# Kernel tuning notes

Hardware: AMD Instinct MI355X
Metric: run time of the kernel (lower is better)

## Reference

```python
import jax, jax.numpy as jnp
import numpy as np

EPS = 1e-5

def _fake_quant(w, axis):
    # symmetric int8 fake-quant with straight-through estimator
    s = jnp.max(jnp.abs(w), axis=axis, keepdims=True) / 127.0 + 1e-8
    q = jnp.clip(jnp.round(w / s), -127.0, 127.0) * s
    return w + jax.lax.stop_gradient(q - w)

def _qconv1x1(x, w, b):
    # x: [B, C_in, Q, H, W]; w: [C_out, C_in] (1x1 kernel); weight fake-quantized
    wq = _fake_quant(w, axis=1)
    return jnp.einsum('bcqhw,oc->boqhw', x, wq) + b[None, :, None, None, None]

def setup_inputs() -> dict:
    key = jax.random.key(0)
    ks = jax.random.split(key, 12)
    B, C, Q, H, W = 8, 256, 4, 40, 40
    x = jax.random.normal(ks[0], (B, C, Q, H, W), dtype=jnp.float32)
    scale = 1.0 / np.sqrt(C)
    Wq = jax.random.normal(ks[1], (C, C), dtype=jnp.float32) * scale
    Wk = jax.random.normal(ks[2], (C, C), dtype=jnp.float32) * scale
    Wv = jax.random.normal(ks[3], (C, C), dtype=jnp.float32) * scale
    Wp = jax.random.normal(ks[4], (C, C), dtype=jnp.float32) * scale
    bq = jnp.zeros((C,), jnp.float32)
    bk = jnp.zeros((C,), jnp.float32)
    bv = jnp.zeros((C,), jnp.float32)
    bp = jnp.zeros((C,), jnp.float32)
    gamma = jnp.ones((C,), jnp.float32)
    beta = jnp.zeros((C,), jnp.float32)
    return {"x": x, "Wq": Wq, "bq": bq, "Wk": Wk, "bk": bk,
            "Wv": Wv, "bv": bv, "Wp": Wp, "bp": bp,
            "gamma": gamma, "beta": beta}

def reference(x, Wq, bq, Wk, bk, Wv, bv, Wp, bp, gamma, beta):
    B, C, Q, H, W = x.shape
    q = _qconv1x1(x, Wq, bq)
    k = _qconv1x1(x, Wk, bk)
    v = _qconv1x1(x, Wv, bv)
    # per-rotation channel attention: [B, Q=4, C, H*W]
    qh = q.reshape(B, C, Q, H * W).transpose(0, 2, 1, 3)
    kh = k.reshape(B, C, Q, H * W).transpose(0, 2, 1, 3)
    vh = v.reshape(B, C, Q, H * W).transpose(0, 2, 1, 3)
    scale = 1.0 / jnp.sqrt(jnp.float32(C // 4))
    attn = jnp.einsum('bqcn,bqdn->bqcd', qh, kh) * scale  # [B,4,C,C]
    attn = jax.nn.softmax(attn, axis=-1)
    out = jnp.einsum('bqcd,bqdn->bqcn', attn, vh)  # [B,4,C,HW]
    out = out.transpose(0, 2, 1, 3).reshape(B, C, Q, H, W)
    out = _qconv1x1(out, Wp, bp)
    # IQBN: per-channel batchnorm with int8 fake-quantized gamma
    mean = jnp.mean(out, axis=(0, 2, 3, 4), keepdims=True)
    var = jnp.var(out, axis=(0, 2, 3, 4), keepdims=True)
    g = _fake_quant(gamma, axis=None)[None, :, None, None, None]
    b = beta[None, :, None, None, None]
    out = (out - mean) * jax.lax.rsqrt(var + EPS) * g + b
    return out
```

## Files before the change

kernel.cpp:

```cpp
#include <hip/hip_runtime.h>
#include <math.h>

#define BB 8
#define CCH 256
#define QQ 4
#define NN 1600
#define BQN 32
#define SP 51200
#define EPSF 1e-5f

typedef __attribute__((ext_vector_type(8))) short bf16x8;
typedef __attribute__((ext_vector_type(4))) float f32x4;

static __device__ inline ushort f2bf(float f) {
  union { float f; unsigned u; } v; v.f = f;
  return (ushort)((v.u + 0x7fffu + ((v.u >> 16) & 1u)) >> 16);
}
static __device__ inline float bf2f(ushort u) {
  union { unsigned u; float f; } v; v.u = ((unsigned)u) << 16;
  return v.f;
}
static __device__ inline void gld16(const ushort* g, ushort* l) {
  __builtin_amdgcn_global_load_lds(
      (const __attribute__((address_space(1))) unsigned int*)g,
      (__attribute__((address_space(3))) unsigned int*)l, 16, 0, 0);
}

__global__ void quant_weights_kernel(const float* Wq, const float* Wk,
                                     const float* Wv, const float* Wp,
                                     const float* gamma,
                                     ushort* wq, ushort* wk, ushort* wvT, ushort* wp,
                                     float* gq, float* r) {
  __shared__ float red[256];
  int blk = blockIdx.x;
  int tid = threadIdx.x;
  if (blk < 1024) {
    int mat = blk >> 8;
    int row = blk & 255;
    const float* W = (mat == 0) ? Wq : (mat == 1) ? Wk : (mat == 2) ? Wv : Wp;
    float w = W[row * 256 + tid];
    red[tid] = fabsf(w);
    __syncthreads();
    for (int s = 128; s > 0; s >>= 1) {
      if (tid < s) red[tid] = fmaxf(red[tid], red[tid + s]);
      __syncthreads();
    }
    float s = red[0] / 127.0f + 1e-8f;
    float q = fminf(fmaxf(rintf(w / s), -127.0f), 127.0f) * s;
    ushort qb = f2bf(q);
    if (mat == 0)      wq[row * 256 + tid] = qb;
    else if (mat == 1) wk[row * 256 + tid] = qb;
    else if (mat == 2) wvT[tid * 256 + row] = qb;
    else               wp[row * 256 + tid] = qb;
  } else {
    float g = gamma[tid];
    red[tid] = fabsf(g);
    __syncthreads();
    for (int s = 128; s > 0; s >>= 1) {
      if (tid < s) red[tid] = fmaxf(red[tid], red[tid + s]);
      __syncthreads();
    }
    float s = red[0] / 127.0f + 1e-8f;
    gq[tid] = fminf(fmaxf(rintf(g / s), -127.0f), 127.0f) * s;
    for (int i = tid; i < BQN * 256; i += 256) r[i] = 0.f;
  }
}

__global__ __launch_bounds__(256)
void prep_kernel(const float* __restrict__ x, ushort* __restrict__ xb,
                 ushort* __restrict__ xT, float* __restrict__ r) {
  int bqi = blockIdx.z, b = bqi >> 2, q = bqi & 3;
  int s0 = blockIdx.x * 64, c0 = blockIdx.y * 64;
  __shared__ ushort lT[64 * 66];
  int tid = threadIdx.x;
  int c = tid >> 2, nch = (tid & 3) * 16;
  const float* xp = x + ((size_t)(b * CCH + c0 + c) * QQ + q) * NN + s0 + nch;
  union { ushort u[16]; int4 v[2]; } nb;
  float s = 0.f;
#pragma unroll
  for (int j = 0; j < 4; j++) {
    float4 f = ((const float4*)xp)[j];
    s += f.x + f.y + f.z + f.w;
    nb.u[j * 4 + 0] = f2bf(f.x);
    nb.u[j * 4 + 1] = f2bf(f.y);
    nb.u[j * 4 + 2] = f2bf(f.z);
    nb.u[j * 4 + 3] = f2bf(f.w);
    lT[c * 66 + nch + j * 4 + 0] = nb.u[j * 4 + 0];
    lT[c * 66 + nch + j * 4 + 1] = nb.u[j * 4 + 1];
    lT[c * 66 + nch + j * 4 + 2] = nb.u[j * 4 + 2];
    lT[c * 66 + nch + j * 4 + 3] = nb.u[j * 4 + 3];
  }
  ushort* xbp = xb + (size_t)bqi * (CCH * NN) + (size_t)(c0 + c) * NN + s0 + nch;
  *(int4*)xbp = nb.v[0];
  *((int4*)xbp + 1) = nb.v[1];
  s += __shfl_down(s, 2);
  s += __shfl_down(s, 1);
  if ((tid & 3) == 0) atomicAdd(&r[bqi * 256 + c0 + c], s);
  __syncthreads();
  int n = tid >> 2, cch = (tid & 3) * 16;
  union { ushort u[16]; int4 v[2]; } o;
#pragma unroll
  for (int i = 0; i < 16; i++) o.u[i] = lT[(cch + i) * 66 + n];
  ushort* dst = xT + (size_t)(bqi * NN + s0 + n) * CCH + c0 + cch;
  *(int4*)dst = o.v[0];
  *((int4*)dst + 1) = o.v[1];
}

__global__ __launch_bounds__(256)
void gram_kernel(const ushort* __restrict__ xb, ushort* __restrict__ Gh,
                 ushort* __restrict__ Gl) {
  __shared__ __align__(16) char smem[32768];
  float* lC = (float*)smem;
  int z = blockIdx.z;
  int mBase = blockIdx.y * 128, nBase = blockIdx.x * 128;
  int tid = threadIdx.x, wave = tid >> 6, lane = tid & 63;
  int wm = wave >> 1, wn = wave & 1;
  int col = lane & 15, quad = lane >> 4;
  int srow = tid >> 2, skc = (tid & 3) * 8;
  const ushort* X = xb + (size_t)z * (CCH * NN);
  const ushort* gA  = X + (size_t)(mBase + srow) * NN + skc;
  const ushort* gA2 = gA + (size_t)64 * NN;
  const ushort* gB  = X + (size_t)(nBase + srow) * NN + skc;
  const ushort* gB2 = gB + (size_t)64 * NN;
  ushort* sA1[2]; ushort* sA2[2]; ushort* sB1[2]; ushort* sB2[2];
#pragma unroll
  for (int b = 0; b < 2; b++) {
    ushort* lAb = (ushort*)(smem + b * 16384);
    ushort* lBb = (ushort*)(smem + b * 16384 + 8192);
    sA1[b] = &lAb[srow * 32 + skc];
    sA2[b] = &lAb[(64 + srow) * 32 + skc];
    sB1[b] = &lBb[srow * 32 + skc];
    sB2[b] = &lBb[(64 + srow) * 32 + skc];
  }
  f32x4 acc[4][4];
#pragma unroll
  for (int i = 0; i < 4; i++)
#pragma unroll
    for (int j = 0; j < 4; j++) acc[i][j] = (f32x4){0.f, 0.f, 0.f, 0.f};

  const int nIter = NN / 32;
  gld16(gA, sA1[0]); gld16(gA2, sA2[0]); gld16(gB, sB1[0]); gld16(gB2, sB2[0]);
  for (int it = 0; it < nIter; ++it) {
    int cur = it & 1;
    __syncthreads();
    if (it + 1 < nIter) {
      int kt = (it + 1) << 5, nxt = cur ^ 1;
      gld16(gA + kt, sA1[nxt]); gld16(gA2 + kt, sA2[nxt]);
      gld16(gB + kt, sB1[nxt]); gld16(gB2 + kt, sB2[nxt]);
    }
    const ushort* lAc = (const ushort*)(smem + cur * 16384);
    const ushort* lBc = (const ushort*)(smem + cur * 16384 + 8192);
    bf16x8 af[4], bfr[4];
#pragma unroll
    for (int i = 0; i < 4; i++)
      af[i] = *(const bf16x8*)&lAc[(wm * 64 + i * 16 + col) * 32 + quad * 8];
#pragma unroll
    for (int j = 0; j < 4; j++)
      bfr[j] = *(const bf16x8*)&lBc[(wn * 64 + j * 16 + col) * 32 + quad * 8];
#pragma unroll
    for (int i = 0; i < 4; i++)
#pragma unroll
      for (int j = 0; j < 4; j++)
        acc[i][j] = __builtin_amdgcn_mfma_f32_16x16x32_bf16(af[i], bfr[j], acc[i][j], 0, 0, 0);
  }
  __syncthreads();
  float* lCw = lC + wave * 16 * 68;
  int mW = mBase + wm * 64, nW = nBase + wn * 64;
#pragma unroll
  for (int i = 0; i < 4; i++) {
#pragma unroll
    for (int j = 0; j < 4; j++)
#pragma unroll
      for (int rg = 0; rg < 4; rg++)
        lCw[(quad * 4 + rg) * 68 + j * 16 + col] = acc[i][j][rg];
    int mrow0 = mW + i * 16;
    int rr = lane & 15, cc = lane >> 4;
    union { ushort u[16]; int4 v[2]; } oh, ol;
#pragma unroll
    for (int t = 0; t < 16; t++) {
      float vfl = lCw[rr * 68 + cc * 16 + t];
      ushort hh = f2bf(vfl);
      oh.u[t] = hh;
      ol.u[t] = f2bf(vfl - bf2f(hh));
    }
    size_t off = (size_t)z * 65536 + (size_t)(mrow0 + rr) * 256 + nW + cc * 16;
    *(int4*)(Gh + off) = oh.v[0];
    *((int4*)(Gh + off) + 1) = oh.v[1];
    *(int4*)(Gl + off) = ol.v[0];
    *((int4*)(Gl + off) + 1) = ol.v[1];
  }
}

template<int MODE>
__global__ __launch_bounds__(256)
void gemm256(const ushort* __restrict__ A, long sA, const ushort* __restrict__ A2,
             const ushort* __restrict__ B, long sB, const ushort* __restrict__ B2,
             void* __restrict__ C1, void* __restrict__ C2, long sC) {
  __shared__ __align__(16) char smem[24576];
  ushort* lA = (ushort*)smem;
  ushort* lB = (ushort*)(smem + 8192);
  ushort* lX = (ushort*)(smem + 16384);
  float* lC = (float*)smem;
  int z = blockIdx.z;
  int mBase = blockIdx.y * 128, nBase = blockIdx.x * 128;
  int tid = threadIdx.x, wave = tid >> 6, lane = tid & 63;
  int wm = wave >> 1, wn = wave & 1;
  int col = lane & 15, quad = lane >> 4;
  int srow = tid >> 2, skc = (tid & 3) * 8;
  const ushort* Az = A + (size_t)z * sA;
  const ushort* Bz = B + (size_t)z * sB;
  const ushort* gA  = Az + (size_t)(mBase + srow) * 256 + skc;
  const ushort* gA2r = gA + 64 * 256;
  const ushort* gB  = Bz + (size_t)(nBase + srow) * 256 + skc;
  const ushort* gB2r = gB + 64 * 256;
  const ushort* gX = nullptr;
  const ushort* gX2 = nullptr;
  if (MODE == 0) {
    const ushort* Xz = B2 + (size_t)z * sB;
    gX = Xz + (size_t)(nBase + srow) * 256 + skc;
    gX2 = gX + 64 * 256;
  } else if (MODE == 1) {
    const ushort* Xz = A2 + (size_t)z * sA;
    gX = Xz + (size_t)(mBase + srow) * 256 + skc;
    gX2 = gX + 64 * 256;
  }
  ushort* dA1 = &lA[srow * 32 + skc]; ushort* dA2 = &lA[(64 + srow) * 32 + skc];
  ushort* dB1 = &lB[srow * 32 + skc]; ushort* dB2 = &lB[(64 + srow) * 32 + skc];
  ushort* dX1 = &lX[srow * 32 + skc]; ushort* dX2 = &lX[(64 + srow) * 32 + skc];

  f32x4 acc[4][4];
#pragma unroll
  for (int i = 0; i < 4; i++)
#pragma unroll
    for (int j = 0; j < 4; j++) acc[i][j] = (f32x4){0.f, 0.f, 0.f, 0.f};

  for (int kt = 0; kt < 256; kt += 32) {
    __syncthreads();
    gld16(gA + kt, dA1); gld16(gA2r + kt, dA2);
    gld16(gB + kt, dB1); gld16(gB2r + kt, dB2);
    if (MODE <= 1) { gld16(gX + kt, dX1); gld16(gX2 + kt, dX2); }
    __syncthreads();
    bf16x8 af[4], bfr[4], xf[4];
#pragma unroll
    for (int i = 0; i < 4; i++)
      af[i] = *(const bf16x8*)&lA[(wm * 64 + i * 16 + col) * 32 + quad * 8];
#pragma unroll
    for (int j = 0; j < 4; j++)
      bfr[j] = *(const bf16x8*)&lB[(wn * 64 + j * 16 + col) * 32 + quad * 8];
    if (MODE == 0) {
#pragma unroll
      for (int j = 0; j < 4; j++)
        xf[j] = *(const bf16x8*)&lX[(wn * 64 + j * 16 + col) * 32 + quad * 8];
    } else if (MODE == 1) {
#pragma unroll
      for (int i = 0; i < 4; i++)
        xf[i] = *(const bf16x8*)&lX[(wm * 64 + i * 16 + col) * 32 + quad * 8];
    }
#pragma unroll
    for (int i = 0; i < 4; i++)
#pragma unroll
      for (int j = 0; j < 4; j++) {
        acc[i][j] = __builtin_amdgcn_mfma_f32_16x16x32_bf16(af[i], bfr[j], acc[i][j], 0, 0, 0);
        if (MODE == 0)
          acc[i][j] = __builtin_amdgcn_mfma_f32_16x16x32_bf16(af[i], xf[j], acc[i][j], 0, 0, 0);
        else if (MODE == 1)
          acc[i][j] = __builtin_amdgcn_mfma_f32_16x16x32_bf16(xf[i], bfr[j], acc[i][j], 0, 0, 0);
      }
  }
  __syncthreads();
  float* lCw = lC + wave * 16 * 68;
  int mW = mBase + wm * 64, nW = nBase + wn * 64;
#pragma unroll
  for (int i = 0; i < 4; i++) {
#pragma unroll
    for (int j = 0; j < 4; j++)
#pragma unroll
      for (int rg = 0; rg < 4; rg++)
        lCw[(quad * 4 + rg) * 68 + j * 16 + col] = acc[i][j][rg];
    int mrow0 = mW + i * 16;
    int rr = lane & 15, cc = lane >> 4;
    if (MODE == 0) {
      union { ushort u[16]; int4 v[2]; } oh, ol;
#pragma unroll
      for (int t = 0; t < 16; t++) {
        float vfl = lCw[rr * 68 + cc * 16 + t];
        ushort hh = f2bf(vfl);
        oh.u[t] = hh;
        ol.u[t] = f2bf(vfl - bf2f(hh));
      }
      size_t off = (size_t)z * sC + (size_t)(mrow0 + rr) * 256 + nW + cc * 16;
      *(int4*)((ushort*)C1 + off) = oh.v[0];
      *((int4*)((ushort*)C1 + off) + 1) = oh.v[1];
      *(int4*)((ushort*)C2 + off) = ol.v[0];
      *((int4*)((ushort*)C2 + off) + 1) = ol.v[1];
    } else if (MODE == 1) {
      float* C = (float*)C1 + (size_t)z * sC + (size_t)(mrow0 + rr) * 256 + nW + cc * 16;
#pragma unroll
      for (int v = 0; v < 4; v++) {
        float4 f;
        f.x = lCw[rr * 68 + cc * 16 + v * 4 + 0];
        f.y = lCw[rr * 68 + cc * 16 + v * 4 + 1];
        f.z = lCw[rr * 68 + cc * 16 + v * 4 + 2];
        f.w = lCw[rr * 68 + cc * 16 + v * 4 + 3];
        *(float4*)(C + v * 4) = f;
      }
    } else if (MODE == 2) {
      int n = nW + lane;
      union { ushort u[16]; int4 v[2]; } o;
#pragma unroll
      for (int t = 0; t < 16; t++) o.u[t] = f2bf(lCw[t * 68 + lane]);
      ushort* C = (ushort*)C1 + (size_t)z * sC + (size_t)n * 256 + mrow0;
      *(int4*)C = o.v[0];
      *((int4*)C + 1) = o.v[1];
    } else {
      union { ushort u[16]; int4 v[2]; } o;
#pragma unroll
      for (int t = 0; t < 16; t++) o.u[t] = f2bf(lCw[rr * 68 + cc * 16 + t]);
      ushort* C = (ushort*)C1 + (size_t)z * sC + (size_t)(mrow0 + rr) * 256 + nW + cc * 16;
      *(int4*)C = o.v[0];
      *((int4*)C + 1) = o.v[1];
    }
  }
}

__global__ void uv_kernel(const ushort* __restrict__ wq, const ushort* __restrict__ wk,
                          const float* __restrict__ r, float* __restrict__ u,
                          float* __restrict__ vv) {
  int bq = blockIdx.x, sel = blockIdx.y, c = threadIdx.x;
  const ushort* W = sel ? wk : wq;
  float s = 0.f;
  for (int i = 0; i < 256; i++) s += bf2f(W[c * 256 + i]) * r[bq * 256 + i];
  (sel ? vv : u)[bq * 256 + c] = s;
}

__global__ void softmax_kernel(const float* __restrict__ S, const float* __restrict__ u,
                               const float* __restrict__ vv, const float* __restrict__ bqv,
                               const float* __restrict__ bkv, const float* __restrict__ bvv,
                               ushort* __restrict__ P, float* __restrict__ pb) {
  int bi = blockIdx.x;
  int bq = bi >> 8, rw = bi & 255;
  int tid = threadIdx.x;
  size_t off = (size_t)bq * 65536 + (size_t)rw * 256 + tid;
  float bqc = bqv[rw], bkd = bkv[tid];
  float val = 0.125f * (S[off] + u[bq * 256 + rw] * bkd + bqc * vv[bq * 256 + tid]
                        + 1600.0f * bqc * bkd);
  __shared__ float red[256];
  red[tid] = val;
  __syncthreads();
  for (int s = 128; s > 0; s >>= 1) {
    if (tid < s) red[tid] = fmaxf(red[tid], red[tid + s]);
    __syncthreads();
  }
  float m = red[0];
  __syncthreads();
  float e = expf(val - m);
  red[tid] = e;
  __syncthreads();
  for (int s = 128; s > 0; s >>= 1) {
    if (tid < s) red[tid] += red[tid + s];
    __syncthreads();
  }
  float p = e / red[0];
  P[off] = f2bf(p);
  __syncthreads();
  red[tid] = p * bvv[tid];
  __syncthreads();
  for (int s = 128; s > 0; s >>= 1) {
    if (tid < s) red[tid] += red[tid + s];
    __syncthreads();
  }
  if (tid == 0) pb[bq * 256 + rw] = red[0];
}

__global__ void bo_kernel(const ushort* __restrict__ wp, const float* __restrict__ pb,
                          const float* __restrict__ bp, float* __restrict__ bo) {
  int bq = blockIdx.x, o = threadIdx.x;
  float s = bp[o];
  for (int c = 0; c < 256; c++) s += bf2f(wp[o * 256 + c]) * pb[bq * 256 + c];
  bo[bq * 256 + o] = s;
}

__global__ __launch_bounds__(256)
void final_kernel(const ushort* __restrict__ Tm, const ushort* __restrict__ xT,
                  const float* __restrict__ bo, float* __restrict__ out,
                  float* __restrict__ part) {
  __shared__ __align__(16) char smem[32768];
  float* lC = (float*)smem;
  __shared__ float psS[2][128];
  __shared__ float psS2[2][128];
  int z = blockIdx.z;
  int mBase = blockIdx.y * 128, nBase = blockIdx.x * 128;
  int tid = threadIdx.x, wave = tid >> 6, lane = tid & 63;
  int wm = wave >> 1, wn = wave & 1;
  int col = lane & 15, quad = lane >> 4;
  int srow = tid >> 2, skc = (tid & 3) * 8;
  const ushort* Az = Tm + (size_t)z * 65536;
  const ushort* Bz = xT + (size_t)z * (NN * 256);
  const ushort* gA  = Az + (size_t)(mBase + srow) * 256 + skc;
  const ushort* gA2 = gA + 64 * 256;
  int br1 = nBase + srow;      br1 = br1 < NN ? br1 : NN - 1;
  int br2 = nBase + 64 + srow; br2 = br2 < NN ? br2 : NN - 1;
  const ushort* gB  = Bz + (size_t)br1 * 256 + skc;
  const ushort* gB2 = Bz + (size_t)br2 * 256 + skc;
  ushort* sA1[2]; ushort* sA2[2]; ushort* sB1[2]; ushort* sB2[2];
#pragma unroll
  for (int b = 0; b < 2; b++) {
    ushort* lAb = (ushort*)(smem + b * 16384);
    ushort* lBb = (ushort*)(smem + b * 16384 + 8192);
    sA1[b] = &lAb[srow * 32 + skc];
    sA2[b] = &lAb[(64 + srow) * 32 + skc];
    sB1[b] = &lBb[srow * 32 + skc];
    sB2[b] = &lBb[(64 + srow) * 32 + skc];
  }
  f32x4 acc[4][4];
#pragma unroll
  for (int i = 0; i < 4; i++)
#pragma unroll
    for (int j = 0; j < 4; j++) acc[i][j] = (f32x4){0.f, 0.f, 0.f, 0.f};

  const int nIter = 8;
  gld16(gA, sA1[0]); gld16(gA2, sA2[0]); gld16(gB, sB1[0]); gld16(gB2, sB2[0]);
  for (int it = 0; it < nIter; ++it) {
    int cur = it & 1;
    __syncthreads();
    if (it + 1 < nIter) {
      int kt = (it + 1) << 5, nxt = cur ^ 1;
      gld16(gA + kt, sA1[nxt]); gld16(gA2 + kt, sA2[nxt]);
      gld16(gB + kt, sB1[nxt]); gld16(gB2 + kt, sB2[nxt]);
    }
    const ushort* lAc = (const ushort*)(smem + cur * 16384);
    const ushort* lBc = (const ushort*)(smem + cur * 16384 + 8192);
    bf16x8 af[4], bfr[4];
#pragma unroll
    for (int i = 0; i < 4; i++)
      af[i] = *(const bf16x8*)&lAc[(wm * 64 + i * 16 + col) * 32 + quad * 8];
#pragma unroll
    for (int j = 0; j < 4; j++)
      bfr[j] = *(const bf16x8*)&lBc[(wn * 64 + j * 16 + col) * 32 + quad * 8];
#pragma unroll
    for (int i = 0; i < 4; i++)
#pragma unroll
      for (int j = 0; j < 4; j++)
        acc[i][j] = __builtin_amdgcn_mfma_f32_16x16x32_bf16(af[i], bfr[j], acc[i][j], 0, 0, 0);
  }
  __syncthreads();
  float* lCw = lC + wave * 16 * 68;
  int mW = mBase + wm * 64, nW = nBase + wn * 64;
  int b = z >> 2, q = z & 3;
#pragma unroll
  for (int i = 0; i < 4; i++) {
#pragma unroll
    for (int j = 0; j < 4; j++)
#pragma unroll
      for (int rg = 0; rg < 4; rg++)
        lCw[(quad * 4 + rg) * 68 + j * 16 + col] = acc[i][j][rg];
    int mrow0 = mW + i * 16;
    int rr = lane & 15, cc = lane >> 4;
    int n0 = nW + cc * 16;
    float bi = bo[(size_t)z * 256 + mrow0 + rr];
    float ls = 0.f, ls2 = 0.f;
    if (n0 < NN) {
      float* C = out + (size_t)b * (CCH * QQ * NN)
               + (size_t)(mrow0 + rr) * (QQ * NN) + (size_t)q * NN + n0;
#pragma unroll
      for (int v = 0; v < 4; v++) {
        float4 f;
        f.x = lCw[rr * 68 + cc * 16 + v * 4 + 0] + bi;
        f.y = lCw[rr * 68 + cc * 16 + v * 4 + 1] + bi;
        f.z = lCw[rr * 68 + cc * 16 + v * 4 + 2] + bi;
        f.w = lCw[rr * 68 + cc * 16 + v * 4 + 3] + bi;
        *(float4*)(C + v * 4) = f;
        ls  += f.x + f.y + f.z + f.w;
        ls2 += f.x * f.x + f.y * f.y + f.z * f.z + f.w * f.w;
      }
    }
    ls  += __shfl_down(ls, 32);  ls  += __shfl_down(ls, 16);
    ls2 += __shfl_down(ls2, 32); ls2 += __shfl_down(ls2, 16);
    if (lane < 16) {
      psS[wn][wm * 64 + i * 16 + lane] = ls;
      psS2[wn][wm * 64 + i * 16 + lane] = ls2;
    }
  }
  __syncthreads();
  if (tid < 128) {
    float s  = psS[0][tid] + psS[1][tid];
    float s2 = psS2[0][tid] + psS2[1][tid];
    int slot = z * 13 + blockIdx.x;
    part[(size_t)slot * 256 + mBase + tid] = s;
    part[416 * 256 + (size_t)slot * 256 + mBase + tid] = s2;
  }
}

__global__ void stats2_kernel(const float* __restrict__ part, float* __restrict__ st) {
  int o = blockIdx.x;
  int tid = threadIdx.x;
  float s = 0.f, s2 = 0.f;
  for (int x = tid; x < 416; x += 256) {
    s  += part[(size_t)x * 256 + o];
    s2 += part[416 * 256 + (size_t)x * 256 + o];
  }
  __shared__ float rs[256], rs2[256];
  rs[tid] = s; rs2[tid] = s2;
  __syncthreads();
  for (int t = 128; t > 0; t >>= 1) {
    if (tid < t) { rs[tid] += rs[tid + t]; rs2[tid] += rs2[tid + t]; }
    __syncthreads();
  }
  if (tid == 0) {
    float inv = 1.0f / (float)(BQN * NN);
    float mean = rs[0] * inv;
    float var = rs2[0] * inv - mean * mean;
    st[o] = mean;
    st[CCH + o] = var;
  }
}

__global__ __launch_bounds__(256)
void bn_kernel(float* __restrict__ out, const float* __restrict__ st,
               const float* __restrict__ gq, const float* __restrict__ beta) {
  size_t i4 = (size_t)blockIdx.x * 256 + threadIdx.x;
  int o = (int)((i4 / 1600) & 255);
  float mean = st[o];
  float g = rsqrtf(st[CCH + o] + EPSF) * gq[o];
  float be = beta[o];
  float4 f = ((const float4*)out)[i4];
  f.x = (f.x - mean) * g + be;
  f.y = (f.y - mean) * g + be;
  f.z = (f.z - mean) * g + be;
  f.w = (f.w - mean) * g + be;
  ((float4*)out)[i4] = f;
}

extern "C" void kernel_launch(void* const* d_in, const int* in_sizes, int n_in,
                              void* d_out, int out_size, void* d_ws, size_t ws_size,
                              hipStream_t stream) {
  const float* x     = (const float*)d_in[0];
  const float* Wq    = (const float*)d_in[1];
  const float* bq    = (const float*)d_in[2];
  const float* Wk    = (const float*)d_in[3];
  const float* bk    = (const float*)d_in[4];
  const float* Wv    = (const float*)d_in[5];
  const float* bv    = (const float*)d_in[6];
  const float* Wp    = (const float*)d_in[7];
  const float* bp    = (const float*)d_in[8];
  const float* gamma = (const float*)d_in[9];
  const float* beta  = (const float*)d_in[10];
  float* out = (float*)d_out;

  ushort* h    = (ushort*)d_ws;
  ushort* wq   = h;
  ushort* wk   = wq + 65536;
  ushort* wp   = wk + 65536;
  ushort* wvT  = wp + 65536;
  ushort* xb   = wvT + 65536;
  ushort* xT   = xb + (size_t)BQN * CCH * NN;
  ushort* Gh   = xT + (size_t)BQN * CCH * NN;
  ushort* Gl   = Gh + (size_t)BQN * 65536;
  ushort* M1h  = Gl + (size_t)BQN * 65536;
  ushort* M1l  = M1h + (size_t)BQN * 65536;
  ushort* P    = M1l + (size_t)BQN * 65536;
  ushort* N1t  = P + (size_t)BQN * 65536;
  ushort* Tm   = N1t + (size_t)BQN * 65536;
  float*  S    = (float*)(Tm + (size_t)BQN * 65536);
  float*  r    = S + (size_t)BQN * 65536;
  float*  u    = r + 8192;
  float*  vv   = u + 8192;
  float*  pb   = vv + 8192;
  float*  bo   = pb + 8192;
  float*  gq   = bo + 8192;
  float*  st   = gq + 256;
  float*  part = st + 512;

  quant_weights_kernel<<<1025, 256, 0, stream>>>(Wq, Wk, Wv, Wp, gamma,
                                                 wq, wk, wvT, wp, gq, r);
  prep_kernel<<<dim3(NN / 64, CCH / 64, BQN), 256, 0, stream>>>(x, xb, xT, r);
  uv_kernel<<<dim3(BQN, 2), 256, 0, stream>>>(wq, wk, r, u, vv);
  gram_kernel<<<dim3(2, 2, BQN), 256, 0, stream>>>(xb, Gh, Gl);
  gemm256<0><<<dim3(2, 2, BQN), 256, 0, stream>>>(
      wq, 0, nullptr, Gh, 65536, Gl, M1h, M1l, 65536);
  gemm256<1><<<dim3(2, 2, BQN), 256, 0, stream>>>(
      M1h, 65536, M1l, wk, 0, nullptr, S, nullptr, 65536);
  softmax_kernel<<<BQN * CCH, 256, 0, stream>>>(S, u, vv, bq, bk, bv, P, pb);
  gemm256<2><<<dim3(2, 2, BQN), 256, 0, stream>>>(
      P, 65536, nullptr, wvT, 0, nullptr, N1t, nullptr, 65536);
  gemm256<3><<<dim3(2, 2, BQN), 256, 0, stream>>>(
      wp, 0, nullptr, N1t, 65536, nullptr, Tm, nullptr, 65536);
  bo_kernel<<<BQN, 256, 0, stream>>>(wp, pb, bp, bo);
  final_kernel<<<dim3(13, 2, BQN), 256, 0, stream>>>(Tm, xT, bo, out, part);
  stats2_kernel<<<CCH, 256, 0, stream>>>(part, st);
  bn_kernel<<<(BB * CCH * QQ * NN / 4) / 256, 256, 0, stream>>>(out, st, gq, beta);
}
```

Before: 285.9 us.

## Compute batchnorm stats analytically from Gram matrix and split Gram over K

Measured after the change: 314.5 us. +10.0%, slower.

```diff
diff --git a/kernel.cpp b/kernel.cpp
--- a/kernel.cpp
+++ b/kernel.cpp
@@ -30,7 +30,7 @@
                                      const float* Wv, const float* Wp,
                                      const float* gamma,
                                      ushort* wq, ushort* wk, ushort* wvT, ushort* wp,
-                                     float* gq, float* r) {
+                                     float* gq, float* r, float* diagacc, float* tracc) {
   __shared__ float red[256];
   int blk = blockIdx.x;
   int tid = threadIdx.x;
@@ -62,7 +62,9 @@
     }
     float s = red[0] / 127.0f + 1e-8f;
     gq[tid] = fminf(fmaxf(rintf(g / s), -127.0f), 127.0f) * s;
-    for (int i = tid; i < BQN * 256; i += 256) r[i] = 0.f;
+    for (int i = tid; i < BQN * 256; i += 256) {
+      r[i] = 0.f; diagacc[i] = 0.f; tracc[i] = 0.f;
+    }
   }
 }
 
@@ -80,15 +82,15 @@
 #pragma unroll
   for (int j = 0; j < 4; j++) {
     float4 f = ((const float4*)xp)[j];
-    s += f.x + f.y + f.z + f.w;
     nb.u[j * 4 + 0] = f2bf(f.x);
     nb.u[j * 4 + 1] = f2bf(f.y);
     nb.u[j * 4 + 2] = f2bf(f.z);
     nb.u[j * 4 + 3] = f2bf(f.w);
-    lT[c * 66 + nch + j * 4 + 0] = nb.u[j * 4 + 0];
-    lT[c * 66 + nch + j * 4 + 1] = nb.u[j * 4 + 1];
-    lT[c * 66 + nch + j * 4 + 2] = nb.u[j * 4 + 2];
-    lT[c * 66 + nch + j * 4 + 3] = nb.u[j * 4 + 3];
+#pragma unroll
+    for (int t = 0; t < 4; t++) {
+      s += bf2f(nb.u[j * 4 + t]);
+      lT[c * 66 + nch + j * 4 + t] = nb.u[j * 4 + t];
+    }
   }
   ushort* xbp = xb + (size_t)bqi * (CCH * NN) + (size_t)(c0 + c) * NN + s0 + nch;
   *(int4*)xbp = nb.v[0];
@@ -107,17 +109,18 @@
 }
 
 __global__ __launch_bounds__(256)
-void gram_kernel(const ushort* __restrict__ xb, ushort* __restrict__ Gh,
-                 ushort* __restrict__ Gl) {
+void gram_part_kernel(const ushort* __restrict__ xb, float* __restrict__ Gp) {
   __shared__ __align__(16) char smem[32768];
-  float* lC = (float*)smem;
   int z = blockIdx.z;
+  int bq = z & 31, chunk = z >> 5;
+  int kbase = chunk * 416;
+  int Kc = 1600 - kbase; if (Kc > 416) Kc = 416;
   int mBase = blockIdx.y * 128, nBase = blockIdx.x * 128;
   int tid = threadIdx.x, wave = tid >> 6, lane = tid & 63;
   int wm = wave >> 1, wn = wave & 1;
   int col = lane & 15, quad = lane >> 4;
   int srow = tid >> 2, skc = (tid & 3) * 8;
-  const ushort* X = xb + (size_t)z * (CCH * NN);
+  const ushort* X = xb + (size_t)bq * (CCH * NN) + kbase;
   const ushort* gA  = X + (size_t)(mBase + srow) * NN + skc;
   const ushort* gA2 = gA + (size_t)64 * NN;
   const ushort* gB  = X + (size_t)(nBase + srow) * NN + skc;
@@ -138,7 +141,7 @@
 #pragma unroll
     for (int j = 0; j < 4; j++) acc[i][j] = (f32x4){0.f, 0.f, 0.f, 0.f};
 
-  const int nIter = NN / 32;
+  int nIter = Kc >> 5;
   gld16(gA, sA1[0]); gld16(gA2, sA2[0]); gld16(gB, sB1[0]); gld16(gB2, sB2[0]);
   for (int it = 0; it < nIter; ++it) {
     int cur = it & 1;
@@ -163,31 +166,45 @@
       for (int j = 0; j < 4; j++)
         acc[i][j] = __builtin_amdgcn_mfma_f32_16x16x32_bf16(af[i], bfr[j], acc[i][j], 0, 0, 0);
   }
-  __syncthreads();
-  float* lCw = lC + wave * 16 * 68;
-  int mW = mBase + wm * 64, nW = nBase + wn * 64;
-#pragma unroll
-  for (int i = 0; i < 4; i++) {
+  float* G = Gp + (size_t)z * 65536;
+#pragma unroll
+  for (int i = 0; i < 4; i++)
 #pragma unroll
     for (int j = 0; j < 4; j++)
 #pragma unroll
-      for (int rg = 0; rg < 4; rg++)
-        lCw[(quad * 4 + rg) * 68 + j * 16 + col] = acc[i][j][rg];
-    int mrow0 = mW + i * 16;
-    int rr = lane & 15, cc = lane >> 4;
-    union { ushort u[16]; int4 v[2]; } oh, ol;
-#pragma unroll
-    for (int t = 0; t < 16; t++) {
-      float vfl = lCw[rr * 68 + cc * 16 + t];
-      ushort hh = f2bf(vfl);
-      oh.u[t] = hh;
-      ol.u[t] = f2bf(vfl - bf2f(hh));
-    }
-    size_t off = (size_t)z * 65536 + (size_t)(mrow0 + rr) * 256 + nW + cc * 16;
-    *(int4*)(Gh + off) = oh.v[0];
-    *((int4*)(Gh + off) + 1) = oh.v[1];
-    *(int4*)(Gl + off) = ol.v[0];
-    *((int4*)(Gl + off) + 1) = ol.v[1];
+      for (int rg = 0; rg < 4; rg++) {
+        int row = mBase + wm * 64 + i * 16 + quad * 4 + rg;
+        int cl  = nBase + wn * 64 + j * 16 + col;
+        G[row * 256 + cl] = acc[i][j][rg];
+      }
+}
+
+__global__ __launch_bounds__(256)
+void gram_reduce_kernel(const float* __restrict__ Gp, ushort* __restrict__ Gh,
+                        ushort* __restrict__ Gl) {
+  int bq = blockIdx.x, tid = threadIdx.x;
+  const size_t cs = (size_t)32 * 65536;
+  for (int k = 0; k < 32; k++) {
+    size_t f8 = (size_t)(tid + k * 256) * 8;
+    size_t base = (size_t)bq * 65536 + f8;
+    union { ushort u[8]; int4 v; } oh, ol;
+#pragma unroll
+    for (int t = 0; t < 8; t += 4) {
+      float4 a = *(const float4*)(Gp + base + t);
+      float4 b = *(const float4*)(Gp + cs + base + t);
+      float4 c = *(const float4*)(Gp + 2 * cs + base + t);
+      float4 d = *(const float4*)(Gp + 3 * cs + base + t);
+      float v0 = a.x + b.x + c.x + d.x;
+      float v1 = a.y + b.y + c.y + d.y;
+      float v2 = a.z + b.z + c.z + d.z;
+      float v3 = a.w + b.w + c.w + d.w;
+      ushort h0 = f2bf(v0), h1 = f2bf(v1), h2 = f2bf(v2), h3 = f2bf(v3);
+      oh.u[t] = h0; oh.u[t + 1] = h1; oh.u[t + 2] = h2; oh.u[t + 3] = h3;
+      ol.u[t] = f2bf(v0 - bf2f(h0)); ol.u[t + 1] = f2bf(v1 - bf2f(h1));
+      ol.u[t + 2] = f2bf(v2 - bf2f(h2)); ol.u[t + 3] = f2bf(v3 - bf2f(h3));
+    }
+    *(int4*)(Gh + base) = oh.v;
+    *(int4*)(Gl + base) = ol.v;
   }
 }
 
@@ -381,13 +398,120 @@
 }
 
 __global__ __launch_bounds__(256)
+void tgt_kernel(const ushort* __restrict__ Tm, const ushort* __restrict__ Gh,
+                const ushort* __restrict__ Gl, const float* __restrict__ r,
+                float* __restrict__ diagacc, float* __restrict__ tracc) {
+  __shared__ __align__(16) char smem[24576];
+  ushort* lA = (ushort*)smem;
+  ushort* lB = (ushort*)(smem + 8192);
+  ushort* lX = (ushort*)(smem + 16384);
+  float* lC = (float*)smem;
+  int z = blockIdx.z;
+  int mBase = blockIdx.y * 128, nBase = blockIdx.x * 128;
+  int tid = threadIdx.x, wave = tid >> 6, lane = tid & 63;
+  int wm = wave >> 1, wn = wave & 1;
+  int col = lane & 15, quad = lane >> 4;
+  int srow = tid >> 2, skc = (tid & 3) * 8;
+  const ushort* Az = Tm + (size_t)z * 65536;
+  const ushort* Bz = Gh + (size_t)z * 65536;
+  const ushort* Xz = Gl + (size_t)z * 65536;
+  const ushort* gA  = Az + (size_t)(mBase + srow) * 256 + skc;
+  const ushort* gA2r = gA + 64 * 256;
+  const ushort* gB  = Bz + (size_t)(nBase + srow) * 256 + skc;
+  const ushort* gB2r = gB + 64 * 256;
+  const ushort* gX  = Xz + (size_t)(nBase + srow) * 256 + skc;
+  const ushort* gX2 = gX + 64 * 256;
+  ushort* dA1 = &lA[srow * 32 + skc]; ushort* dA2 = &lA[(64 + srow) * 32 + skc];
+  ushort* dB1 = &lB[srow * 32 + skc]; ushort* dB2 = &lB[(64 + srow) * 32 + skc];
+  ushort* dX1 = &lX[srow * 32 + skc]; ushort* dX2 = &lX[(64 + srow) * 32 + skc];
+
+  f32x4 acc[4][4];
+#pragma unroll
+  for (int i = 0; i < 4; i++)
+#pragma unroll
+    for (int j = 0; j < 4; j++) acc[i][j] = (f32x4){0.f, 0.f, 0.f, 0.f};
+
+  for (int kt = 0; kt < 256; kt += 32) {
+    __syncthreads();
+    gld16(gA + kt, dA1); gld16(gA2r + kt, dA2);
+    gld16(gB + kt, dB1); gld16(gB2r + kt, dB2);
+    gld16(gX + kt, dX1); gld16(gX2 + kt, dX2);
+    __syncthreads();
+    bf16x8 af[4], bfr[4], xf[4];
+#pragma unroll
+    for (int i = 0; i < 4; i++)
+      af[i] = *(const bf16x8*)&lA[(wm * 64 + i * 16 + col) * 32 + quad * 8];
+#pragma unroll
+    for (int j = 0; j < 4; j++) {
+      bfr[j] = *(const bf16x8*)&lB[(wn * 64 + j * 16 + col) * 32 + quad * 8];
+      xf[j]  = *(const bf16x8*)&lX[(wn * 64 + j * 16 + col) * 32 + quad * 8];
+    }
+#pragma unroll
+    for (int i = 0; i < 4; i++)
+#pragma unroll
+      for (int j = 0; j < 4; j++) {
+        acc[i][j] = __builtin_amdgcn_mfma_f32_16x16x32_bf16(af[i], bfr[j], acc[i][j], 0, 0, 0);
+        acc[i][j] = __builtin_amdgcn_mfma_f32_16x16x32_bf16(af[i], xf[j], acc[i][j], 0, 0, 0);
+      }
+  }
+  __syncthreads();
+  float* lCw = lC + wave * 16 * 68;
+  int mW = mBase + wm * 64, nW = nBase + wn * 64;
+#pragma unroll
+  for (int i = 0; i < 4; i++) {
+#pragma unroll
+    for (int j = 0; j < 4; j++)
+#pragma unroll
+      for (int rg = 0; rg < 4; rg++)
+        lCw[(quad * 4 + rg) * 68 + j * 16 + col] = acc[i][j][rg];
+    int mrow0 = mW + i * 16;
+    int rr = lane & 15, cc = lane >> 4;
+    const ushort* Trow = Tm + (size_t)z * 65536 + (size_t)(mrow0 + rr) * 256 + nW + cc * 16;
+    const float* rrow = r + (size_t)z * 256 + nW + cc * 16;
+    float sd = 0.f, st = 0.f;
+#pragma unroll
+    for (int t = 0; t < 16; t++) {
+      float tv = bf2f(Trow[t]);
+      sd += lCw[rr * 68 + cc * 16 + t] * tv;
+      st += tv * rrow[t];
+    }
+    sd += __shfl_xor(sd, 16); sd += __shfl_xor(sd, 32);
+    st += __shfl_xor(st, 16); st += __shfl_xor(st, 32);
+    if (lane < 16) {
+      atomicAdd(&diagacc[z * 256 + mrow0 + rr], sd);
+      atomicAdd(&tracc[z * 256 + mrow0 + rr], st);
+    }
+  }
+}
+
+__global__ void chanstats_kernel(const float* __restrict__ diagacc,
+                                 const float* __restrict__ tracc,
+                                 const float* __restrict__ bo,
+                                 const float* __restrict__ gq,
+                                 float* __restrict__ stm, float* __restrict__ stg) {
+  int o = threadIdx.x;
+  float sd = 0.f, str = 0.f, sb = 0.f, spt = 0.f, sb2 = 0.f;
+  for (int bq = 0; bq < BQN; bq++) {
+    float d = diagacc[bq * 256 + o];
+    float t = tracc[bq * 256 + o];
+    float b = bo[bq * 256 + o];
+    sd += d; str += t; sb += b; spt += b * t; sb2 += b * b;
+  }
+  float inv = 1.0f / (float)(BQN * NN);
+  float mean = (str + (float)NN * sb) * inv;
+  float e2 = (sd + 2.0f * spt + (float)NN * sb2) * inv;
+  float var = e2 - mean * mean;
+  stm[o] = mean;
+  stg[o] = rsqrtf(var + EPSF) * gq[o];
+}
+
+__global__ __launch_bounds__(256)
 void final_kernel(const ushort* __restrict__ Tm, const ushort* __restrict__ xT,
-                  const float* __restrict__ bo, float* __restrict__ out,
-                  float* __restrict__ part) {
+                  const float* __restrict__ bo, const float* __restrict__ stm,
+                  const float* __restrict__ stg, const float* __restrict__ beta,
+                  float* __restrict__ out) {
   __shared__ __align__(16) char smem[32768];
   float* lC = (float*)smem;
-  __shared__ float psS[2][128];
-  __shared__ float psS2[2][128];
   int z = blockIdx.z;
   int mBase = blockIdx.y * 128, nBase = blockIdx.x * 128;
   int tid = threadIdx.x, wave = tid >> 6, lane = tid & 63;
@@ -457,78 +581,23 @@
     int mrow0 = mW + i * 16;
     int rr = lane & 15, cc = lane >> 4;
     int n0 = nW + cc * 16;
-    float bi = bo[(size_t)z * 256 + mrow0 + rr];
-    float ls = 0.f, ls2 = 0.f;
     if (n0 < NN) {
+      int ch = mrow0 + rr;
+      float g = stg[ch];
+      float rb = (bo[(size_t)z * 256 + ch] - stm[ch]) * g + beta[ch];
       float* C = out + (size_t)b * (CCH * QQ * NN)
-               + (size_t)(mrow0 + rr) * (QQ * NN) + (size_t)q * NN + n0;
+               + (size_t)ch * (QQ * NN) + (size_t)q * NN + n0;
 #pragma unroll
       for (int v = 0; v < 4; v++) {
         float4 f;
-        f.x = lCw[rr * 68 + cc * 16 + v * 4 + 0] + bi;
-        f.y = lCw[rr * 68 + cc * 16 + v * 4 + 1] + bi;
-        f.z = lCw[rr * 68 + cc * 16 + v * 4 + 2] + bi;
-        f.w = lCw[rr * 68 + cc * 16 + v * 4 + 3] + bi;
+        f.x = lCw[rr * 68 + cc * 16 + v * 4 + 0] * g + rb;
+        f.y = lCw[rr * 68 + cc * 16 + v * 4 + 1] * g + rb;
+        f.z = lCw[rr * 68 + cc * 16 + v * 4 + 2] * g + rb;
+        f.w = lCw[rr * 68 + cc * 16 + v * 4 + 3] * g + rb;
         *(float4*)(C + v * 4) = f;
-        ls  += f.x + f.y + f.z + f.w;
-        ls2 += f.x * f.x + f.y * f.y + f.z * f.z + f.w * f.w;
       }
     }
-    ls  += __shfl_down(ls, 32);  ls  += __shfl_down(ls, 16);
-    ls2 += __shfl_down(ls2, 32); ls2 += __shfl_down(ls2, 16);
-    if (lane < 16) {
-      psS[wn][wm * 64 + i * 16 + lane] = ls;
-      psS2[wn][wm * 64 + i * 16 + lane] = ls2;
-    }
-  }
-  __syncthreads();
-  if (tid < 128) {
-    float s  = psS[0][tid] + psS[1][tid];
-    float s2 = psS2[0][tid] + psS2[1][tid];
-    int slot = z * 13 + blockIdx.x;
-    part[(size_t)slot * 256 + mBase + tid] = s;
-    part[416 * 256 + (size_t)slot * 256 + mBase + tid] = s2;
-  }
-}
-
-__global__ void stats2_kernel(const float* __restrict__ part, float* __restrict__ st) {
-  int o = blockIdx.x;
-  int tid = threadIdx.x;
-  float s = 0.f, s2 = 0.f;
-  for (int x = tid; x < 416; x += 256) {
-    s  += part[(size_t)x * 256 + o];
-    s2 += part[416 * 256 + (size_t)x * 256 + o];
-  }
-  __shared__ float rs[256], rs2[256];
-  rs[tid] = s; rs2[tid] = s2;
-  __syncthreads();
-  for (int t = 128; t > 0; t >>= 1) {
-    if (tid < t) { rs[tid] += rs[tid + t]; rs2[tid] += rs2[tid + t]; }
-    __syncthreads();
-  }
-  if (tid == 0) {
-    float inv = 1.0f / (float)(BQN * NN);
-    float mean = rs[0] * inv;
-    float var = rs2[0] * inv - mean * mean;
-    st[o] = mean;
-    st[CCH + o] = var;
-  }
-}
-
-__global__ __launch_bounds__(256)
-void bn_kernel(float* __restrict__ out, const float* __restrict__ st,
-               const float* __restrict__ gq, const float* __restrict__ beta) {
-  size_t i4 = (size_t)blockIdx.x * 256 + threadIdx.x;
-  int o = (int)((i4 / 1600) & 255);
-  float mean = st[o];
-  float g = rsqrtf(st[CCH + o] + EPSF) * gq[o];
-  float be = beta[o];
-  float4 f = ((const float4*)out)[i4];
-  f.x = (f.x - mean) * g + be;
-  f.y = (f.y - mean) * g + be;
-  f.z = (f.z - mean) * g + be;
-  f.w = (f.w - mean) * g + be;
-  ((float4*)out)[i4] = f;
+  }
 }
 
 extern "C" void kernel_launch(void* const* d_in, const int* in_sizes, int n_in,
@@ -562,20 +631,24 @@
   ushort* N1t  = P + (size_t)BQN * 65536;
   ushort* Tm   = N1t + (size_t)BQN * 65536;
   float*  S    = (float*)(Tm + (size_t)BQN * 65536);
-  float*  r    = S + (size_t)BQN * 65536;
+  float*  Gp   = S + (size_t)BQN * 65536;
+  float*  r    = Gp + (size_t)4 * BQN * 65536;
   float*  u    = r + 8192;
   float*  vv   = u + 8192;
   float*  pb   = vv + 8192;
   float*  bo   = pb + 8192;
-  float*  gq   = bo + 8192;
-  float*  st   = gq + 256;
-  float*  part = st + 512;
+  float*  diagacc = bo + 8192;
+  float*  tracc   = diagacc + 8192;
+  float*  gq   = tracc + 8192;
+  float*  stm  = gq + 256;
+  float*  stg  = stm + 256;
 
   quant_weights_kernel<<<1025, 256, 0, stream>>>(Wq, Wk, Wv, Wp, gamma,
-                                                 wq, wk, wvT, wp, gq, r);
+                                                 wq, wk, wvT, wp, gq, r, diagacc, tracc);
   prep_kernel<<<dim3(NN / 64, CCH / 64, BQN), 256, 0, stream>>>(x, xb, xT, r);
   uv_kernel<<<dim3(BQN, 2), 256, 0, stream>>>(wq, wk, r, u, vv);
-  gram_kernel<<<dim3(2, 2, BQN), 256, 0, stream>>>(xb, Gh, Gl);
+  gram_part_kernel<<<dim3(2, 2, 4 * BQN), 256, 0, stream>>>(xb, Gp);
+  gram_reduce_kernel<<<BQN, 256, 0, stream>>>(Gp, Gh, Gl);
   gemm256<0><<<dim3(2, 2, BQN), 256, 0, stream>>>(
       wq, 0, nullptr, Gh, 65536, Gl, M1h, M1l, 65536);
   gemm256<1><<<dim3(2, 2, BQN), 256, 0, stream>>>(
@@ -586,7 +659,7 @@
   gemm256<3><<<dim3(2, 2, BQN), 256, 0, stream>>>(
       wp, 0, nullptr, N1t, 65536, nullptr, Tm, nullptr, 65536);
   bo_kernel<<<BQN, 256, 0, stream>>>(wp, pb, bp, bo);
-  final_kernel<<<dim3(13, 2, BQN), 256, 0, stream>>>(Tm, xT, bo, out, part);
-  stats2_kernel<<<CCH, 256, 0, stream>>>(part, st);
-  bn_kernel<<<(BB * CCH * QQ * NN / 4) / 256, 256, 0, stream>>>(out, st, gq, beta);
-}
+  tgt_kernel<<<dim3(2, 2, BQN), 256, 0, stream>>>(Tm, Gh, Gl, r, diagacc, tracc);
+  chanstats_kernel<<<1, 256, 0, stream>>>(diagacc, tracc, bo, gq, stm, stg);
+  final_kernel<<<dim3(13, 2, BQN), 256, 0, stream>>>(Tm, xT, bo, stm, stg, beta, out);
+}
```
